# Kernel tuning notes

Hardware: AMD Instinct MI355X
Metric: run time of the kernel (lower is better)

Reference implementation:

```python
import jax, jax.numpy as jnp
import numpy as np
import math

N_EXPERTS = 32
K_SEL = 4
IN_C = 1024
OUT_C = 1024
BATCH = 4096


def setup_inputs() -> dict:
    key = jax.random.key(0)
    kx, ki, kw = jax.random.split(key, 3)
    x = jax.random.normal(kx, (BATCH, IN_C), dtype=jnp.float32)
    idx = jax.random.randint(ki, (BATCH, K_SEL), 0, N_EXPERTS, dtype=jnp.int64)
    # xavier_uniform with gain=sqrt(2) (relu) on (n, in_c, out_c):
    # fan_in = in_c, fan_out = out_c for each expert's 2D slice
    gain = math.sqrt(2.0)
    bound = gain * math.sqrt(6.0 / (IN_C + OUT_C))
    w = jax.random.uniform(kw, (N_EXPERTS, IN_C, OUT_C), dtype=jnp.float32,
                           minval=-bound, maxval=bound)
    b = jnp.zeros((N_EXPERTS, 1, OUT_C), dtype=jnp.float32)
    return {"x": x, "idx": idx, "w": w, "b": b}


def reference(x, idx, w, b):
    # Per-sample selection of k of n FC layers:
    # out[bat, k, o] = relu( x[bat] @ w[idx[bat,k]] + b[idx[bat,k]] )
    # Computed densely over all n experts then gathered, which avoids
    # materializing a (B, K, in_c, out_c) gathered-weight tensor.
    y_all = jnp.einsum('bi,nio->bno', x, w) + b[:, 0, :][None]  # (B, n, out_c)
    out = jnp.take_along_axis(y_all, idx[:, :, None], axis=1)   # (B, K, out_c)
    return jax.nn.relu(out)
```

## Files before the change

kernel.cpp:

```cpp
#include <hip/hip_runtime.h>
#include <hip/hip_bf16.h>

#define N_EXPERTS 32
#define K_SEL 4
#define IN_C 1024
#define OUT_C 1024
#define BATCH 4096
#define NTOK (BATCH * K_SEL)

#define BM 128
#define BN 128
#define BK 64
#define MAX_TILES (N_EXPERTS + NTOK / BM)

#define WT_ELEMS (N_EXPERTS * IN_C * OUT_C)
#define XB_ELEMS (BATCH * IN_C)
#define CTRL_OFF_BYTES ((size_t)WT_ELEMS * 2 + (size_t)XB_ELEMS * 2)

#define WS_NTILES 0
#define WS_TABLE 8
#define WS_ROWLIST (WS_TABLE + MAX_TILES * 4)
#define CTRL_INTS (WS_ROWLIST + NTOK)
#define WS_COUNTS (CTRL_INTS)
#define WS_CURSOR (CTRL_INTS + 32)

typedef __attribute__((ext_vector_type(4))) float f32x4;
typedef __attribute__((ext_vector_type(8))) short bf16x8;
typedef __attribute__((ext_vector_type(8))) unsigned short u16x8;

__device__ __forceinline__ unsigned short f2bf(float f) {
    union { float f; unsigned u; } v; v.f = f;
    unsigned r = v.u + 0x7fffu + ((v.u >> 16) & 1u);
    return (unsigned short)(r >> 16);
}

__device__ __forceinline__ void gload16(const void* g, void* l) {
    __builtin_amdgcn_global_load_lds(
        (const __attribute__((address_space(1))) unsigned int*)g,
        (__attribute__((address_space(3))) unsigned int*)l, 16, 0, 0);
}


#define XCONV_B0 1
#define XCONV_NB (XB_ELEMS / 2048)
#define WCONV_B0 (XCONV_B0 + XCONV_NB)
#define WCONV_NB (N_EXPERTS * 256)
#define PREP_NWG (WCONV_B0 + WCONV_NB)

__global__ __launch_bounds__(256)
void prep_kernel(const float* __restrict__ x, const float* __restrict__ w,
                 const int* __restrict__ idx,
                 unsigned short* __restrict__ xb, unsigned short* __restrict__ wt,
                 int* __restrict__ ctrl) {
    const int bid = blockIdx.x;
    const int t = threadIdx.x;

    if (bid >= WCONV_B0) {
        __shared__ float tb[64][65];
        const int b = bid - WCONV_B0;
        const int e = b >> 8;
        const int tile = b & 255;
        const int kb = (tile >> 4) << 6;
        const int nb = (tile & 15) << 6;
        const float* src = w + (size_t)e * (IN_C * OUT_C);
        const int r = t >> 2, c0 = (t & 3) << 4;
        #pragma unroll
        for (int u = 0; u < 4; ++u) {
            f32x4 v = *(const f32x4*)(src + (size_t)(kb + r) * OUT_C + nb + c0 + (u << 2));
            tb[r][c0 + (u << 2) + 0] = v.x;
            tb[r][c0 + (u << 2) + 1] = v.y;
            tb[r][c0 + (u << 2) + 2] = v.z;
            tb[r][c0 + (u << 2) + 3] = v.w;
        }
        __syncthreads();
        unsigned short* dst = wt + (size_t)e * (IN_C * OUT_C) + (size_t)(nb + r) * IN_C + kb + c0;
        u16x8 o0, o1;
        #pragma unroll
        for (int j = 0; j < 8; ++j) o0[j] = f2bf(tb[c0 + j][r]);
        #pragma unroll
        for (int j = 0; j < 8; ++j) o1[j] = f2bf(tb[c0 + 8 + j][r]);
        *(u16x8*)dst = o0;
        *(u16x8*)(dst + 8) = o1;
    } else if (bid >= XCONV_B0) {
        int i = ((bid - XCONV_B0) * 256 + t) << 3;
        f32x4 v0 = *(const f32x4*)(x + i);
        f32x4 v1 = *(const f32x4*)(x + i + 4);
        u16x8 o;
        o[0] = f2bf(v0.x); o[1] = f2bf(v0.y); o[2] = f2bf(v0.z); o[3] = f2bf(v0.w);
        o[4] = f2bf(v1.x); o[5] = f2bf(v1.y); o[6] = f2bf(v1.z); o[7] = f2bf(v1.w);
        *(u16x8*)(xb + i) = o;
    } else {
        __shared__ int cnt[N_EXPERTS], base[N_EXPERTS], tbase[N_EXPERTS];
        if (t < N_EXPERTS) cnt[t] = 0;
        __syncthreads();
        #pragma unroll 4
        for (int i = 0; i < NTOK / 256; ++i) {
            int e = idx[i * 256 + t] & (N_EXPERTS - 1);
            atomicAdd(&cnt[e], 1);
        }
        __syncthreads();
        if (t == 0) {
            int off = 0, tiles = 0;
            for (int e = 0; e < N_EXPERTS; ++e) {
                base[e] = off;
                tbase[e] = tiles;
                int c = cnt[e];
                tiles += (c + BM - 1) / BM;
                off += c;
            }
            ctrl[WS_NTILES] = tiles;
        }
        __syncthreads();
        if (t < N_EXPERTS) {
            int c = cnt[t], off = base[t], tt = tbase[t];
            for (int u = 0; u < c; u += BM, ++tt) {
                ctrl[WS_TABLE + tt * 4 + 0] = t;
                ctrl[WS_TABLE + tt * 4 + 1] = off + u;
                ctrl[WS_TABLE + tt * 4 + 2] = (c - u) < BM ? (c - u) : BM;
            }
            cnt[t] = off;
        }
        __syncthreads();
        #pragma unroll 4
        for (int i = 0; i < NTOK / 256; ++i) {
            int s = i * 256 + t;
            int e = idx[s] & (N_EXPERTS - 1);
            int p = atomicAdd(&cnt[e], 1);
            ctrl[WS_ROWLIST + p] = s;
        }
    }
}


__global__ __launch_bounds__(256, 3)
void gemm_kernel(const unsigned short* __restrict__ xb,
                 const unsigned short* __restrict__ wt,
                 const float* __restrict__ bias,
                 const int* __restrict__ ctrl,
                 float* __restrict__ out) {
    const int swz = ((int)blockIdx.x & 7) * ((MAX_TILES * 8) >> 3) + ((int)blockIdx.x >> 3);
    const int tileIdx = swz >> 3;
    const int ntiles = ctrl[WS_NTILES];
    if (tileIdx >= ntiles) return;
    const int e     = ctrl[WS_TABLE + tileIdx * 4 + 0];
    const int list0 = ctrl[WS_TABLE + tileIdx * 4 + 1];
    const int nrows = ctrl[WS_TABLE + tileIdx * 4 + 2];
    const int n0 = (swz & 7) * BN;

    __shared__ unsigned short As[BM][BK];
    __shared__ unsigned short Bs[BN][BK];
    __shared__ int rowtok[BM];

    const int t = threadIdx.x;
    const int lane = t & 63, w = t >> 6;

    if (t < BM) {
        int r = t < nrows ? t : nrows - 1;
        rowtok[t] = ctrl[WS_ROWLIST + list0 + r];
    }
    __syncthreads();

    const int cg = (lane & 7) ^ (lane >> 3);
    const unsigned short* asrc[4];
    const unsigned short* bsrc[4];
    #pragma unroll
    for (int i = 0; i < 4; ++i) {
        int row = (w << 5) + (i << 3) + (lane >> 3);
        asrc[i] = xb + (size_t)(rowtok[row] >> 2) * IN_C + (cg << 3);
        bsrc[i] = wt + (size_t)e * (IN_C * OUT_C) + (size_t)(n0 + row) * IN_C + (cg << 3);
    }

    const int wr = (t >> 7) & 1;
    const int wc = (t >> 6) & 1;
    const int lrow = lane & 15, lq = lane >> 4;
    const int fo0 = ((lq) ^ (lrow & 7)) << 4;
    const int fo1 = ((4 + lq) ^ (lrow & 7)) << 4;
    const char* aB = (const char*)&As[wr * 64 + lrow][0];
    const char* bB = (const char*)&Bs[wc * 64 + lrow][0];

    f32x4 acc[4][4];
    #pragma unroll
    for (int m = 0; m < 4; ++m)
        #pragma unroll
        for (int n = 0; n < 4; ++n) acc[m][n] = (f32x4)0.f;

    for (int k0 = 0; k0 < IN_C; k0 += BK) {
        __syncthreads();
        #pragma unroll
        for (int i = 0; i < 4; ++i) {
            gload16(asrc[i] + k0, &As[(w << 5) + (i << 3)][0]);
            gload16(bsrc[i] + k0, &Bs[(w << 5) + (i << 3)][0]);
        }
        __syncthreads();

        #pragma unroll
        for (int kk = 0; kk < 2; ++kk) {
            const int fo = kk ? fo1 : fo0;
            bf16x8 a[4], b[4];
            #pragma unroll
            for (int m = 0; m < 4; ++m) a[m] = *(const bf16x8*)(aB + m * 2048 + fo);
            #pragma unroll
            for (int n = 0; n < 4; ++n) b[n] = *(const bf16x8*)(bB + n * 2048 + fo);
            #pragma unroll
            for (int m = 0; m < 4; ++m)
                #pragma unroll
                for (int n = 0; n < 4; ++n)
                    acc[m][n] = __builtin_amdgcn_mfma_f32_16x16x32_bf16(a[m], b[n], acc[m][n], 0, 0, 0);
        }
    }

    #pragma unroll
    for (int m = 0; m < 4; ++m) {
        #pragma unroll
        for (int j = 0; j < 4; ++j) {
            int row = wr * 64 + m * 16 + lq * 4 + j;
            if (row < nrows) {
                int s = rowtok[row];
                float* orow = out + (size_t)s * OUT_C;
                #pragma unroll
                for (int n = 0; n < 4; ++n) {
                    int col = n0 + wc * 64 + n * 16 + lrow;
                    float vv = acc[m][n][j] + bias[e * OUT_C + col];
                    orow[col] = vv > 0.f ? vv : 0.f;
                }
            }
        }
    }
}


__global__ void count_kernel(const int* __restrict__ idx, int* __restrict__ ctrl) {
    int s = blockIdx.x * blockDim.x + threadIdx.x;
    if (s < NTOK) atomicAdd(&ctrl[WS_COUNTS + (idx[s] & (N_EXPERTS - 1))], 1);
}

__global__ void scan_kernel(int* __restrict__ ctrl) {
    if (threadIdx.x != 0) return;
    int off = 0, tiles = 0;
    for (int e = 0; e < N_EXPERTS; ++e) {
        int c = ctrl[WS_COUNTS + e];
        ctrl[WS_CURSOR + e] = off;
        for (int t = 0; t < c; t += BM) {
            ctrl[WS_TABLE + tiles * 4 + 0] = e;
            ctrl[WS_TABLE + tiles * 4 + 1] = off + t;
            ctrl[WS_TABLE + tiles * 4 + 2] = (c - t) < BM ? (c - t) : BM;
            ++tiles;
        }
        off += c;
    }
    ctrl[WS_NTILES] = tiles;
}

__global__ void scatter_kernel(const int* __restrict__ idx, int* __restrict__ ctrl) {
    int s = blockIdx.x * blockDim.x + threadIdx.x;
    if (s < NTOK) {
        int e = idx[s] & (N_EXPERTS - 1);
        int p = atomicAdd(&ctrl[WS_CURSOR + e], 1);
        ctrl[WS_ROWLIST + p] = s;
    }
}

__global__ __launch_bounds__(256, 2)
void gemm_f32_kernel(const float* __restrict__ x, const float* __restrict__ w,
                     const float* __restrict__ bias, const int* __restrict__ ctrl,
                     float* __restrict__ out) {
    int ntiles = ctrl[WS_NTILES];
    if ((int)blockIdx.x >= ntiles) return;
    const int e     = ctrl[WS_TABLE + blockIdx.x * 4 + 0];
    const int list0 = ctrl[WS_TABLE + blockIdx.x * 4 + 1];
    const int nrows = ctrl[WS_TABLE + blockIdx.x * 4 + 2];
    const int n0 = blockIdx.y * BN;

    __shared__ unsigned short As2[BM][40];
    __shared__ unsigned short Bs2[BN][40];
    __shared__ int rowtok[BM];

    const int t = threadIdx.x;
    if (t < BM) {
        int r = t < nrows ? t : nrows - 1;
        rowtok[t] = ctrl[WS_ROWLIST + list0 + r];
    }
    __syncthreads();

    const int arow = t >> 1, acol0 = (t & 1) * 16;
    const int brow = t >> 3, bcol0 = (t & 7) * 16;
    const float* xbase = x + (size_t)(rowtok[arow] >> 2) * IN_C + acol0;
    const float* wbase = w + (size_t)e * IN_C * OUT_C + (size_t)brow * OUT_C + n0 + bcol0;

    const int lane = t & 63, wid = t >> 6;
    const int wr = wid >> 1, wc = wid & 1;
    const int lrow = lane & 15, lq = lane >> 4;

    f32x4 acc[4][4];
    #pragma unroll
    for (int m = 0; m < 4; ++m)
        #pragma unroll
        for (int n = 0; n < 4; ++n) acc[m][n] = (f32x4)0.f;

    for (int k0 = 0; k0 < IN_C; k0 += 32) {
        __syncthreads();
        #pragma unroll
        for (int u = 0; u < 4; ++u) {
            f32x4 v = *(const f32x4*)(xbase + k0 + 4 * u);
            ushort4 pk;
            pk.x = f2bf(v.x); pk.y = f2bf(v.y); pk.z = f2bf(v.z); pk.w = f2bf(v.w);
            *(ushort4*)&As2[arow][acol0 + 4 * u] = pk;
        }
        #pragma unroll
        for (int u = 0; u < 4; ++u) {
            f32x4 v = *(const f32x4*)(wbase + (size_t)k0 * OUT_C + 4 * u);
            Bs2[bcol0 + 4 * u + 0][brow] = f2bf(v.x);
            Bs2[bcol0 + 4 * u + 1][brow] = f2bf(v.y);
            Bs2[bcol0 + 4 * u + 2][brow] = f2bf(v.z);
            Bs2[bcol0 + 4 * u + 3][brow] = f2bf(v.w);
        }
        __syncthreads();

        bf16x8 a[4], b[4];
        #pragma unroll
        for (int m = 0; m < 4; ++m) a[m] = *(const bf16x8*)&As2[wr * 64 + m * 16 + lrow][lq * 8];
        #pragma unroll
        for (int n = 0; n < 4; ++n) b[n] = *(const bf16x8*)&Bs2[wc * 64 + n * 16 + lrow][lq * 8];
        #pragma unroll
        for (int m = 0; m < 4; ++m)
            #pragma unroll
            for (int n = 0; n < 4; ++n)
                acc[m][n] = __builtin_amdgcn_mfma_f32_16x16x32_bf16(a[m], b[n], acc[m][n], 0, 0, 0);
    }

    #pragma unroll
    for (int m = 0; m < 4; ++m) {
        #pragma unroll
        for (int j = 0; j < 4; ++j) {
            int row = wr * 64 + m * 16 + lq * 4 + j;
            if (row < nrows) {
                int s = rowtok[row];
                float* orow = out + (size_t)s * OUT_C;
                #pragma unroll
                for (int n = 0; n < 4; ++n) {
                    int col = n0 + wc * 64 + n * 16 + lrow;
                    float vv = acc[m][n][j] + bias[e * OUT_C + col];
                    orow[col] = vv > 0.f ? vv : 0.f;
                }
            }
        }
    }
}


extern "C" void kernel_launch(void* const* d_in, const int* in_sizes, int n_in,
                              void* d_out, int out_size, void* d_ws, size_t ws_size,
                              hipStream_t stream) {
    const float* x    = (const float*)d_in[0];
    const int*   idx  = (const int*)d_in[1];
    const float* w    = (const float*)d_in[2];
    const float* bias = (const float*)d_in[3];
    float* out = (float*)d_out;

    const size_t need = CTRL_OFF_BYTES + (size_t)(CTRL_INTS + 64) * sizeof(int);
    if (ws_size >= need) {
        unsigned short* wt = (unsigned short*)d_ws;
        unsigned short* xb = (unsigned short*)((char*)d_ws + (size_t)WT_ELEMS * 2);
        int* ctrl = (int*)((char*)d_ws + CTRL_OFF_BYTES);

        prep_kernel<<<PREP_NWG, 256, 0, stream>>>(x, w, idx, xb, wt, ctrl);
        gemm_kernel<<<MAX_TILES * 8, 256, 0, stream>>>(xb, wt, bias, ctrl, out);
    } else {
        int* ctrl = (int*)d_ws;
        hipMemsetAsync(ctrl, 0, (CTRL_INTS + 64) * sizeof(int), stream);
        count_kernel<<<NTOK / 256, 256, 0, stream>>>(idx, ctrl);
        scan_kernel<<<1, 64, 0, stream>>>(ctrl);
        scatter_kernel<<<NTOK / 256, 256, 0, stream>>>(idx, ctrl);
        dim3 grid(MAX_TILES, OUT_C / BN);
        gemm_f32_kernel<<<grid, 256, 0, stream>>>(x, w, bias, ctrl, out);
    }
}
```

Measured before the change: 119.5 us.

## Pipeline weight transpose-convert over four k-tiles with swizzled bf16 LDS buffers

The weight fp32-to-bf16 transpose now has each workgroup handle four 64x64 k-tiles. It double-buffers a swizzled bf16 LDS tile and issues the next global loads while the previous tile is read out, instead of one padded fp32 tile per block. Weight and x loads switch to nontemporal loads, and GEMM output stores become nontemporal stores, to reduce cache pollution from streaming data. The block ordering in the prep kernel changes so the weight blocks come first. The intent is to hide load latency and halve LDS footprint in the bandwidth-bound conversion, at the cost of fewer, longer-running workgroups.

```diff
diff --git a/kernel.cpp b/kernel.cpp
--- a/kernel.cpp
+++ b/kernel.cpp
@@ -41,11 +41,36 @@
 }
 
 
-#define XCONV_B0 1
+#define WCONV_B0 1
+#define WCONV_NB 2048
+#define XCONV_B0 (WCONV_B0 + WCONV_NB)
 #define XCONV_NB (XB_ELEMS / 2048)
-#define WCONV_B0 (XCONV_B0 + XCONV_NB)
-#define WCONV_NB (N_EXPERTS * 256)
-#define PREP_NWG (WCONV_B0 + WCONV_NB)
+#define PREP_NWG (XCONV_B0 + XCONV_NB)
+
+__device__ __forceinline__ void wr_tile(unsigned short* tbb, int wa0, int wa1,
+                                        f32x4 R0, f32x4 R1, f32x4 R2, f32x4 R3) {
+    u16x8 q0, q1;
+    q0[0] = f2bf(R0.x); q0[1] = f2bf(R0.y); q0[2] = f2bf(R0.z); q0[3] = f2bf(R0.w);
+    q0[4] = f2bf(R1.x); q0[5] = f2bf(R1.y); q0[6] = f2bf(R1.z); q0[7] = f2bf(R1.w);
+    q1[0] = f2bf(R2.x); q1[1] = f2bf(R2.y); q1[2] = f2bf(R2.z); q1[3] = f2bf(R2.w);
+    q1[4] = f2bf(R3.x); q1[5] = f2bf(R3.y); q1[6] = f2bf(R3.z); q1[7] = f2bf(R3.w);
+    *(u16x8*)&tbb[wa0] = q0;
+    *(u16x8*)&tbb[wa1] = q1;
+}
+
+__device__ __forceinline__ void rd_store(const unsigned short* tbb, int rr, int cc0,
+                                         unsigned short* dst) {
+    u16x8 o0, o1;
+    const int rlo = rr & 7, rhi = rr >> 3;
+    #pragma unroll
+    for (int j = 0; j < 8; ++j) {
+        const int sw = ((rhi ^ (j & 7)) << 3) + rlo;
+        o0[j] = tbb[(cc0 + j) * 64 + sw];
+        o1[j] = tbb[(cc0 + 8 + j) * 64 + sw];
+    }
+    *(u16x8*)dst = o0;
+    *(u16x8*)(dst + 8) = o1;
+}
 
 __global__ __launch_bounds__(256)
 void prep_kernel(const float* __restrict__ x, const float* __restrict__ w,
@@ -55,40 +80,58 @@
     const int bid = blockIdx.x;
     const int t = threadIdx.x;
 
-    if (bid >= WCONV_B0) {
-        __shared__ float tb[64][65];
-        const int b = bid - WCONV_B0;
-        const int e = b >> 8;
-        const int tile = b & 255;
-        const int kb = (tile >> 4) << 6;
-        const int nb = (tile & 15) << 6;
-        const float* src = w + (size_t)e * (IN_C * OUT_C);
-        const int r = t >> 2, c0 = (t & 3) << 4;
-        #pragma unroll
-        for (int u = 0; u < 4; ++u) {
-            f32x4 v = *(const f32x4*)(src + (size_t)(kb + r) * OUT_C + nb + c0 + (u << 2));
-            tb[r][c0 + (u << 2) + 0] = v.x;
-            tb[r][c0 + (u << 2) + 1] = v.y;
-            tb[r][c0 + (u << 2) + 2] = v.z;
-            tb[r][c0 + (u << 2) + 3] = v.w;
-        }
-        __syncthreads();
-        unsigned short* dst = wt + (size_t)e * (IN_C * OUT_C) + (size_t)(nb + r) * IN_C + kb + c0;
-        u16x8 o0, o1;
-        #pragma unroll
-        for (int j = 0; j < 8; ++j) o0[j] = f2bf(tb[c0 + j][r]);
-        #pragma unroll
-        for (int j = 0; j < 8; ++j) o1[j] = f2bf(tb[c0 + 8 + j][r]);
-        *(u16x8*)dst = o0;
-        *(u16x8*)(dst + 8) = o1;
-    } else if (bid >= XCONV_B0) {
+    if (bid >= XCONV_B0) {
         int i = ((bid - XCONV_B0) * 256 + t) << 3;
-        f32x4 v0 = *(const f32x4*)(x + i);
-        f32x4 v1 = *(const f32x4*)(x + i + 4);
+        f32x4 v0 = __builtin_nontemporal_load((const f32x4*)(x + i));
+        f32x4 v1 = __builtin_nontemporal_load((const f32x4*)(x + i + 4));
         u16x8 o;
         o[0] = f2bf(v0.x); o[1] = f2bf(v0.y); o[2] = f2bf(v0.z); o[3] = f2bf(v0.w);
         o[4] = f2bf(v1.x); o[5] = f2bf(v1.y); o[6] = f2bf(v1.z); o[7] = f2bf(v1.w);
         *(u16x8*)(xb + i) = o;
+    } else if (bid >= WCONV_B0) {
+        __shared__ unsigned short tb[2][64 * 64];
+        const int b = bid - WCONV_B0;
+        const int e = b >> 6;
+        const int p = b & 63;
+        const int nb = (p & 15) << 6;
+        const int kb0 = (p >> 4) << 8;
+
+        const int r = t >> 2;
+        const int cs = (t & 3) << 1;
+        const int c0 = (t & 3) << 4;
+        const float* srcb = w + (size_t)e * (IN_C * OUT_C) + (size_t)(kb0 + r) * OUT_C + nb + c0;
+        const int wa0 = r * 64 + (((cs    ) ^ (r & 7)) << 3);
+        const int wa1 = r * 64 + (((cs + 1) ^ (r & 7)) << 3);
+
+        const int rr = t & 63;
+        const int cc0 = (t >> 6) << 4;
+        unsigned short* dstb = wt + (size_t)e * (IN_C * OUT_C) + (size_t)(nb + rr) * IN_C + kb0 + cc0;
+
+        f32x4 a0, a1, a2, a3, b0, b1, b2, b3;
+        #define LDT(kt, R0, R1, R2, R3) { \
+            const float* s_ = srcb + (size_t)((kt) * 64) * OUT_C; \
+            R0 = __builtin_nontemporal_load((const f32x4*)s_); \
+            R1 = __builtin_nontemporal_load((const f32x4*)(s_ + 4)); \
+            R2 = __builtin_nontemporal_load((const f32x4*)(s_ + 8)); \
+            R3 = __builtin_nontemporal_load((const f32x4*)(s_ + 12)); }
+
+        LDT(0, a0, a1, a2, a3);
+        LDT(1, b0, b1, b2, b3);
+        wr_tile(&tb[0][0], wa0, wa1, a0, a1, a2, a3);
+        __syncthreads();
+        wr_tile(&tb[1][0], wa0, wa1, b0, b1, b2, b3);
+        LDT(2, a0, a1, a2, a3);
+        rd_store(&tb[0][0], rr, cc0, dstb + 0 * 64);
+        __syncthreads();
+        wr_tile(&tb[0][0], wa0, wa1, a0, a1, a2, a3);
+        LDT(3, b0, b1, b2, b3);
+        rd_store(&tb[1][0], rr, cc0, dstb + 1 * 64);
+        __syncthreads();
+        wr_tile(&tb[1][0], wa0, wa1, b0, b1, b2, b3);
+        rd_store(&tb[0][0], rr, cc0, dstb + 2 * 64);
+        __syncthreads();
+        rd_store(&tb[1][0], rr, cc0, dstb + 3 * 64);
+        #undef LDT
     } else {
         __shared__ int cnt[N_EXPERTS], base[N_EXPERTS], tbase[N_EXPERTS];
         if (t < N_EXPERTS) cnt[t] = 0;
@@ -221,7 +264,8 @@
                 for (int n = 0; n < 4; ++n) {
                     int col = n0 + wc * 64 + n * 16 + lrow;
                     float vv = acc[m][n][j] + bias[e * OUT_C + col];
-                    orow[col] = vv > 0.f ? vv : 0.f;
+                    vv = vv > 0.f ? vv : 0.f;
+                    __builtin_nontemporal_store(vv, &orow[col]);
                 }
             }
         }
```

Result: slower. 135.8 us (+13.6%).

## Pre-tile and pre-swizzle weights into GEMM tile layout during prep conversion

Applied to the files above, without the earlier changes.

The weight conversion in the prep kernel is rewritten so each block converts 16 full k-rows of one expert to bf16, transposes them through shared memory, and writes them in a blocked layout. That layout matches the GEMM's 128x64 B tile, with the XOR swizzle already applied, so each tile is one contiguous 16KB chunk. The GEMM B loads become fully contiguous per tile instead of 128 strided rows, which should improve coalescing and cache behavior. The prep conversion now uses bigger blocks and a 32KB LDS buffer, with row-contiguous fp32 reads.

```diff
diff --git a/kernel.cpp b/kernel.cpp
--- a/kernel.cpp
+++ b/kernel.cpp
@@ -41,11 +41,11 @@
 }
 
 
-#define XCONV_B0 1
+#define WCONV_B0 1
+#define WCONV_NB (N_EXPERTS * 64)
+#define XCONV_B0 (WCONV_B0 + WCONV_NB)
 #define XCONV_NB (XB_ELEMS / 2048)
-#define WCONV_B0 (XCONV_B0 + XCONV_NB)
-#define WCONV_NB (N_EXPERTS * 256)
-#define PREP_NWG (WCONV_B0 + WCONV_NB)
+#define PREP_NWG (XCONV_B0 + XCONV_NB)
 
 __global__ __launch_bounds__(256)
 void prep_kernel(const float* __restrict__ x, const float* __restrict__ w,
@@ -55,33 +55,7 @@
     const int bid = blockIdx.x;
     const int t = threadIdx.x;
 
-    if (bid >= WCONV_B0) {
-        __shared__ float tb[64][65];
-        const int b = bid - WCONV_B0;
-        const int e = b >> 8;
-        const int tile = b & 255;
-        const int kb = (tile >> 4) << 6;
-        const int nb = (tile & 15) << 6;
-        const float* src = w + (size_t)e * (IN_C * OUT_C);
-        const int r = t >> 2, c0 = (t & 3) << 4;
-        #pragma unroll
-        for (int u = 0; u < 4; ++u) {
-            f32x4 v = *(const f32x4*)(src + (size_t)(kb + r) * OUT_C + nb + c0 + (u << 2));
-            tb[r][c0 + (u << 2) + 0] = v.x;
-            tb[r][c0 + (u << 2) + 1] = v.y;
-            tb[r][c0 + (u << 2) + 2] = v.z;
-            tb[r][c0 + (u << 2) + 3] = v.w;
-        }
-        __syncthreads();
-        unsigned short* dst = wt + (size_t)e * (IN_C * OUT_C) + (size_t)(nb + r) * IN_C + kb + c0;
-        u16x8 o0, o1;
-        #pragma unroll
-        for (int j = 0; j < 8; ++j) o0[j] = f2bf(tb[c0 + j][r]);
-        #pragma unroll
-        for (int j = 0; j < 8; ++j) o1[j] = f2bf(tb[c0 + 8 + j][r]);
-        *(u16x8*)dst = o0;
-        *(u16x8*)(dst + 8) = o1;
-    } else if (bid >= XCONV_B0) {
+    if (bid >= XCONV_B0) {
         int i = ((bid - XCONV_B0) * 256 + t) << 3;
         f32x4 v0 = *(const f32x4*)(x + i);
         f32x4 v1 = *(const f32x4*)(x + i + 4);
@@ -89,6 +63,51 @@
         o[0] = f2bf(v0.x); o[1] = f2bf(v0.y); o[2] = f2bf(v0.z); o[3] = f2bf(v0.w);
         o[4] = f2bf(v1.x); o[5] = f2bf(v1.y); o[6] = f2bf(v1.z); o[7] = f2bf(v1.w);
         *(u16x8*)(xb + i) = o;
+    } else if (bid >= WCONV_B0) {
+        __shared__ unsigned short tbuf[16 * 1024];
+        const int b = bid - WCONV_B0;
+        const int e = b >> 6;
+        const int sub = b & 63;
+        const int kb0 = sub << 4;
+        const float* src = w + ((size_t)e << 20) + ((size_t)kb0 << 10) + (t << 2);
+
+        f32x4 ra[8], rb[8];
+        #pragma unroll
+        for (int j = 0; j < 8; ++j) ra[j] = *(const f32x4*)(src + (j << 10));
+        #pragma unroll
+        for (int j = 0; j < 8; ++j) rb[j] = *(const f32x4*)(src + ((8 + j) << 10));
+        #pragma unroll
+        for (int j = 0; j < 8; ++j) {
+            ushort4 pk;
+            pk.x = f2bf(ra[j].x); pk.y = f2bf(ra[j].y);
+            pk.z = f2bf(ra[j].z); pk.w = f2bf(ra[j].w);
+            *(ushort4*)&tbuf[(j << 10) + (t << 2)] = pk;
+        }
+        #pragma unroll
+        for (int j = 0; j < 8; ++j) {
+            ushort4 pk;
+            pk.x = f2bf(rb[j].x); pk.y = f2bf(rb[j].y);
+            pk.z = f2bf(rb[j].z); pk.w = f2bf(rb[j].w);
+            *(ushort4*)&tbuf[((8 + j) << 10) + (t << 2)] = pk;
+        }
+        __syncthreads();
+
+        const int row = t & 127, cl = t >> 7;
+        const int kp = sub >> 2, q = sub & 3;
+        const int chunk = (q << 1) + cl;
+        const int phys = chunk ^ (row & 7);
+        #pragma unroll
+        for (int np = 0; np < 8; ++np) {
+            const int n = (np << 7) + row;
+            u16x8 o;
+            #pragma unroll
+            for (int j = 0; j < 8; ++j)
+                o[j] = tbuf[(((cl << 3) + j) << 10) + n];
+            unsigned short* dst = wt
+                + ((((size_t)e * 8 + np) * 16 + kp) << 13)
+                + (row << 6) + (phys << 3);
+            *(u16x8*)dst = o;
+        }
     } else {
         __shared__ int cnt[N_EXPERTS], base[N_EXPERTS], tbase[N_EXPERTS];
         if (t < N_EXPERTS) cnt[t] = 0;
@@ -145,7 +164,8 @@
     const int e     = ctrl[WS_TABLE + tileIdx * 4 + 0];
     const int list0 = ctrl[WS_TABLE + tileIdx * 4 + 1];
     const int nrows = ctrl[WS_TABLE + tileIdx * 4 + 2];
-    const int n0 = (swz & 7) * BN;
+    const int np = swz & 7;
+    const int n0 = np * BN;
 
     __shared__ unsigned short As[BM][BK];
     __shared__ unsigned short Bs[BN][BK];
@@ -162,13 +182,15 @@
 
     const int cg = (lane & 7) ^ (lane >> 3);
     const unsigned short* asrc[4];
-    const unsigned short* bsrc[4];
     #pragma unroll
     for (int i = 0; i < 4; ++i) {
         int row = (w << 5) + (i << 3) + (lane >> 3);
         asrc[i] = xb + (size_t)(rowtok[row] >> 2) * IN_C + (cg << 3);
-        bsrc[i] = wt + (size_t)e * (IN_C * OUT_C) + (size_t)(n0 + row) * IN_C + (cg << 3);
-    }
+    }
+    const unsigned short* bsrc[4];
+    #pragma unroll
+    for (int i = 0; i < 4; ++i)
+        bsrc[i] = wt + (((size_t)e * 8 + np) << 17) + (w << 11) + (i << 9) + (lane << 3);
 
     const int wr = (t >> 7) & 1;
     const int wc = (t >> 6) & 1;
@@ -189,7 +211,7 @@
         #pragma unroll
         for (int i = 0; i < 4; ++i) {
             gload16(asrc[i] + k0, &As[(w << 5) + (i << 3)][0]);
-            gload16(bsrc[i] + k0, &Bs[(w << 5) + (i << 3)][0]);
+            gload16(bsrc[i] + (k0 << 7), &Bs[(w << 5) + (i << 3)][0]);
         }
         __syncthreads();
 
```

Result: slower. 130.2 us (+8.9%).

## Fuse weight fp32-to-bf16 transpose conversion into GEMM B-tile loading

Applied to the files above, without the earlier changes.

Drops the separate pass in the prep kernel that converted and transposed all expert weights to bf16 in workspace. The GEMM now loads fp32 weight rows directly into registers, converts them to bf16, and writes them transposed into a swizzled shared-memory layout with matching read offsets. This removes a full read and write of the 128MB weight tensor per call. In exchange, each tile reloads and reconverts fp32 weights (twice the bytes per load), and the loads become synchronous register loads instead of direct-to-LDS loads.

```diff
diff --git a/kernel.cpp b/kernel.cpp
--- a/kernel.cpp
+++ b/kernel.cpp
@@ -13,9 +13,8 @@
 #define BK 64
 #define MAX_TILES (N_EXPERTS + NTOK / BM)
 
-#define WT_ELEMS (N_EXPERTS * IN_C * OUT_C)
 #define XB_ELEMS (BATCH * IN_C)
-#define CTRL_OFF_BYTES ((size_t)WT_ELEMS * 2 + (size_t)XB_ELEMS * 2)
+#define CTRL_OFF_BYTES ((size_t)XB_ELEMS * 2)
 
 #define WS_NTILES 0
 #define WS_TABLE 8
@@ -43,51 +42,21 @@
 
 #define XCONV_B0 1
 #define XCONV_NB (XB_ELEMS / 2048)
-#define WCONV_B0 (XCONV_B0 + XCONV_NB)
-#define WCONV_NB (N_EXPERTS * 256)
-#define PREP_NWG (WCONV_B0 + WCONV_NB)
+#define PREP_NWG (XCONV_B0 + XCONV_NB)
 
 __global__ __launch_bounds__(256)
-void prep_kernel(const float* __restrict__ x, const float* __restrict__ w,
-                 const int* __restrict__ idx,
-                 unsigned short* __restrict__ xb, unsigned short* __restrict__ wt,
-                 int* __restrict__ ctrl) {
+void prep_kernel(const float* __restrict__ x, const int* __restrict__ idx,
+                 unsigned short* __restrict__ xb, int* __restrict__ ctrl) {
     const int bid = blockIdx.x;
     const int t = threadIdx.x;
 
-    if (bid >= WCONV_B0) {
-        __shared__ float tb[64][65];
-        const int b = bid - WCONV_B0;
-        const int e = b >> 8;
-        const int tile = b & 255;
-        const int kb = (tile >> 4) << 6;
-        const int nb = (tile & 15) << 6;
-        const float* src = w + (size_t)e * (IN_C * OUT_C);
-        const int r = t >> 2, c0 = (t & 3) << 4;
-        #pragma unroll
-        for (int u = 0; u < 4; ++u) {
-            f32x4 v = *(const f32x4*)(src + (size_t)(kb + r) * OUT_C + nb + c0 + (u << 2));
-            tb[r][c0 + (u << 2) + 0] = v.x;
-            tb[r][c0 + (u << 2) + 1] = v.y;
-            tb[r][c0 + (u << 2) + 2] = v.z;
-            tb[r][c0 + (u << 2) + 3] = v.w;
-        }
-        __syncthreads();
-        unsigned short* dst = wt + (size_t)e * (IN_C * OUT_C) + (size_t)(nb + r) * IN_C + kb + c0;
-        u16x8 o0, o1;
-        #pragma unroll
-        for (int j = 0; j < 8; ++j) o0[j] = f2bf(tb[c0 + j][r]);
-        #pragma unroll
-        for (int j = 0; j < 8; ++j) o1[j] = f2bf(tb[c0 + 8 + j][r]);
-        *(u16x8*)dst = o0;
-        *(u16x8*)(dst + 8) = o1;
-    } else if (bid >= XCONV_B0) {
+    if (bid >= XCONV_B0) {
         int i = ((bid - XCONV_B0) * 256 + t) << 3;
         f32x4 v0 = *(const f32x4*)(x + i);
         f32x4 v1 = *(const f32x4*)(x + i + 4);
         u16x8 o;
-        o[0] = f2bf(v0.x); o[1] = f2bf(v0.y); o[2] = f2bf(v0.z); o[3] = f2bf(v0.w);
-        o[4] = f2bf(v1.x); o[5] = f2bf(v1.y); o[6] = f2bf(v1.z); o[7] = f2bf(v1.w);
+        o[0] = f2bf(v0[0]); o[1] = f2bf(v0[1]); o[2] = f2bf(v0[2]); o[3] = f2bf(v0[3]);
+        o[4] = f2bf(v1[0]); o[5] = f2bf(v1[1]); o[6] = f2bf(v1[2]); o[7] = f2bf(v1[3]);
         *(u16x8*)(xb + i) = o;
     } else {
         __shared__ int cnt[N_EXPERTS], base[N_EXPERTS], tbase[N_EXPERTS];
@@ -134,7 +103,7 @@
 
 __global__ __launch_bounds__(256, 3)
 void gemm_kernel(const unsigned short* __restrict__ xb,
-                 const unsigned short* __restrict__ wt,
+                 const float* __restrict__ w,
                  const float* __restrict__ bias,
                  const int* __restrict__ ctrl,
                  float* __restrict__ out) {
@@ -152,7 +121,7 @@
     __shared__ int rowtok[BM];
 
     const int t = threadIdx.x;
-    const int lane = t & 63, w = t >> 6;
+    const int lane = t & 63, wv = t >> 6;
 
     if (t < BM) {
         int r = t < nrows ? t : nrows - 1;
@@ -162,21 +131,28 @@
 
     const int cg = (lane & 7) ^ (lane >> 3);
     const unsigned short* asrc[4];
-    const unsigned short* bsrc[4];
     #pragma unroll
     for (int i = 0; i < 4; ++i) {
-        int row = (w << 5) + (i << 3) + (lane >> 3);
+        int row = (wv << 5) + (i << 3) + (lane >> 3);
         asrc[i] = xb + (size_t)(rowtok[row] >> 2) * IN_C + (cg << 3);
-        bsrc[i] = wt + (size_t)e * (IN_C * OUT_C) + (size_t)(n0 + row) * IN_C + (cg << 3);
-    }
+    }
+
+    const int q = t & 31, o = t >> 5;
+    const float* bbase = w + ((size_t)e << 20) + (size_t)(o << 3 << 10) + n0 + (q << 2);
 
     const int wr = (t >> 7) & 1;
     const int wc = (t >> 6) & 1;
     const int lrow = lane & 15, lq = lane >> 4;
-    const int fo0 = ((lq) ^ (lrow & 7)) << 4;
-    const int fo1 = ((4 + lq) ^ (lrow & 7)) << 4;
+    const int afo0 = ((lq) ^ (lrow & 7)) << 4;
+    const int afo1 = ((4 + lq) ^ (lrow & 7)) << 4;
     const char* aB = (const char*)&As[wr * 64 + lrow][0];
     const char* bB = (const char*)&Bs[wc * 64 + lrow][0];
+    int bfo[2][4];
+    #pragma unroll
+    for (int kk = 0; kk < 2; ++kk)
+        #pragma unroll
+        for (int nf = 0; nf < 4; ++nf)
+            bfo[kk][nf] = ((((kk << 2) + lq) ^ (lrow & 7) ^ ((2 * nf + (lrow >> 3)) & 7)) << 4);
 
     f32x4 acc[4][4];
     #pragma unroll
@@ -186,21 +162,33 @@
 
     for (int k0 = 0; k0 < IN_C; k0 += BK) {
         __syncthreads();
-        #pragma unroll
-        for (int i = 0; i < 4; ++i) {
-            gload16(asrc[i] + k0, &As[(w << 5) + (i << 3)][0]);
-            gload16(bsrc[i] + k0, &Bs[(w << 5) + (i << 3)][0]);
+        f32x4 breg[8];
+        const float* bsrc = bbase + ((size_t)k0 << 10);
+        #pragma unroll
+        for (int r = 0; r < 8; ++r)
+            breg[r] = *(const f32x4*)(bsrc + ((size_t)r << 10));
+        #pragma unroll
+        for (int i = 0; i < 4; ++i)
+            gload16(asrc[i] + k0, &As[(wv << 5) + (i << 3)][0]);
+        #pragma unroll
+        for (int j = 0; j < 4; ++j) {
+            const int n = (q << 2) + j;
+            const int phys = o ^ (n & 7) ^ ((n >> 3) & 7);
+            u16x8 ov;
+            #pragma unroll
+            for (int r = 0; r < 8; ++r) ov[r] = f2bf(breg[r][j]);
+            *(u16x8*)&Bs[n][phys << 3] = ov;
         }
         __syncthreads();
 
         #pragma unroll
         for (int kk = 0; kk < 2; ++kk) {
-            const int fo = kk ? fo1 : fo0;
+            const int afo = kk ? afo1 : afo0;
             bf16x8 a[4], b[4];
             #pragma unroll
-            for (int m = 0; m < 4; ++m) a[m] = *(const bf16x8*)(aB + m * 2048 + fo);
-            #pragma unroll
-            for (int n = 0; n < 4; ++n) b[n] = *(const bf16x8*)(bB + n * 2048 + fo);
+            for (int m = 0; m < 4; ++m) a[m] = *(const bf16x8*)(aB + m * 2048 + afo);
+            #pragma unroll
+            for (int n = 0; n < 4; ++n) b[n] = *(const bf16x8*)(bB + n * 2048 + bfo[kk][n]);
             #pragma unroll
             for (int m = 0; m < 4; ++m)
                 #pragma unroll
@@ -303,16 +291,16 @@
         for (int u = 0; u < 4; ++u) {
             f32x4 v = *(const f32x4*)(xbase + k0 + 4 * u);
             ushort4 pk;
-            pk.x = f2bf(v.x); pk.y = f2bf(v.y); pk.z = f2bf(v.z); pk.w = f2bf(v.w);
+            pk.x = f2bf(v[0]); pk.y = f2bf(v[1]); pk.z = f2bf(v[2]); pk.w = f2bf(v[3]);
             *(ushort4*)&As2[arow][acol0 + 4 * u] = pk;
         }
         #pragma unroll
         for (int u = 0; u < 4; ++u) {
             f32x4 v = *(const f32x4*)(wbase + (size_t)k0 * OUT_C + 4 * u);
-            Bs2[bcol0 + 4 * u + 0][brow] = f2bf(v.x);
-            Bs2[bcol0 + 4 * u + 1][brow] = f2bf(v.y);
-            Bs2[bcol0 + 4 * u + 2][brow] = f2bf(v.z);
-            Bs2[bcol0 + 4 * u + 3][brow] = f2bf(v.w);
+            Bs2[bcol0 + 4 * u + 0][brow] = f2bf(v[0]);
+            Bs2[bcol0 + 4 * u + 1][brow] = f2bf(v[1]);
+            Bs2[bcol0 + 4 * u + 2][brow] = f2bf(v[2]);
+            Bs2[bcol0 + 4 * u + 3][brow] = f2bf(v[3]);
         }
         __syncthreads();
 
@@ -359,12 +347,11 @@
 
     const size_t need = CTRL_OFF_BYTES + (size_t)(CTRL_INTS + 64) * sizeof(int);
     if (ws_size >= need) {
-        unsigned short* wt = (unsigned short*)d_ws;
-        unsigned short* xb = (unsigned short*)((char*)d_ws + (size_t)WT_ELEMS * 2);
+        unsigned short* xb = (unsigned short*)d_ws;
         int* ctrl = (int*)((char*)d_ws + CTRL_OFF_BYTES);
 
-        prep_kernel<<<PREP_NWG, 256, 0, stream>>>(x, w, idx, xb, wt, ctrl);
-        gemm_kernel<<<MAX_TILES * 8, 256, 0, stream>>>(xb, wt, bias, ctrl, out);
+        prep_kernel<<<PREP_NWG, 256, 0, stream>>>(x, idx, xb, ctrl);
+        gemm_kernel<<<MAX_TILES * 8, 256, 0, stream>>>(xb, w, bias, ctrl, out);
     } else {
         int* ctrl = (int*)d_ws;
         hipMemsetAsync(ctrl, 0, (CTRL_INTS + 64) * sizeof(int), stream);
```

Result: faster. 105.3 us (-11.9%).
